# Kernel tuning notes

Hardware: AMD Instinct MI355X
Metric: run time of the kernel (lower is better)

The kernel has to match this reference:

```python
import jax, jax.numpy as jnp
import numpy as np

NUM_HEADS = 16
NUM_KV_HEADS = 4
HEAD_DIM = 128
ROPE_THETA = 10000.0


def _rope_cos_sin(T, dim, theta):
    inv_freq = 1.0 / (theta ** (jnp.arange(0, dim, 2, dtype=jnp.float32) / dim))
    freqs = jnp.arange(T, dtype=jnp.float32)[:, None] * inv_freq[None, :]  # (T, dim/2)
    emb = jnp.concatenate([freqs, freqs], axis=-1)  # (T, dim)
    return jnp.cos(emb), jnp.sin(emb)


def _rotate_half(x):
    h = x.shape[-1] // 2
    return jnp.concatenate([-x[..., h:], x[..., :h]], axis=-1)


def _apply_rope(x, cos, sin):
    # x: (B, H, T, D); cos/sin: (T, D)
    return x * cos[None, None] + _rotate_half(x) * sin[None, None]


def setup_inputs() -> dict:
    key = jax.random.key(0)
    ks = jax.random.split(key, 6)
    B, T, H = 2, 2048, 2048
    latent = 256
    kv_dim = NUM_KV_HEADS * HEAD_DIM
    s = 0.02
    return {
        "x": jax.random.normal(ks[0], (B, T, H), jnp.float32),
        "wq": jax.random.normal(ks[1], (H, H), jnp.float32) * s,
        "wkv": jax.random.normal(ks[2], (latent, H), jnp.float32) * s,
        "wk": jax.random.normal(ks[3], (kv_dim, latent), jnp.float32) * s,
        "wv": jax.random.normal(ks[4], (kv_dim, latent), jnp.float32) * s,
        "wo": jax.random.normal(ks[5], (H, H), jnp.float32) * s,
    }


def reference(x, wq, wkv, wk, wv, wo):
    B, T, hidden = x.shape
    nh, nkv, hd = NUM_HEADS, NUM_KV_HEADS, HEAD_DIM

    q = jnp.einsum('bth,dh->btd', x, wq)
    kv_latent = jnp.einsum('bth,lh->btl', x, wkv)
    k = jnp.einsum('btl,dl->btd', kv_latent, wk)
    v = jnp.einsum('btl,dl->btd', kv_latent, wv)

    q = q.reshape(B, T, nh, hd).transpose(0, 2, 1, 3)   # (B, nh, T, hd)
    k = k.reshape(B, T, nkv, hd).transpose(0, 2, 1, 3)  # (B, nkv, T, hd)
    v = v.reshape(B, T, nkv, hd).transpose(0, 2, 1, 3)

    cos, sin = _rope_cos_sin(T, hd, ROPE_THETA)
    q = _apply_rope(q, cos, sin)
    k = _apply_rope(k, cos, sin)

    rep = nh // nkv
    k = jnp.repeat(k, rep, axis=1)  # (B, nh, T, hd)
    v = jnp.repeat(v, rep, axis=1)

    scores = jnp.einsum('bhqd,bhkd->bhqk', q, k) * (1.0 / np.sqrt(hd))
    causal = jnp.triu(jnp.ones((T, T), dtype=bool), k=1)
    scores = jnp.where(causal[None, None], -jnp.inf, scores)
    probs = jax.nn.softmax(scores, axis=-1)
    out = jnp.einsum('bhqk,bhkd->bhqd', probs, v)
    out = out.transpose(0, 2, 1, 3).reshape(B, T, nh * hd)
    return jnp.einsum('btd,hd->bth', out, wo)
```

## Files before the change

### kernel.cpp

```cpp
#include <hip/hip_runtime.h>
#include <hip/hip_bf16.h>
#include <math.h>


#define AS1 __attribute__((address_space(1)))
#define AS3 __attribute__((address_space(3)))
#define QSTRIDE 2304

typedef short bf16x8 __attribute__((ext_vector_type(8)));
typedef float f32x4 __attribute__((ext_vector_type(4)));
typedef float f32x16 __attribute__((ext_vector_type(16)));
typedef unsigned int uint32x2 __attribute__((ext_vector_type(2)));

__device__ __forceinline__ unsigned short f2bf(float x) {
  union { float f; unsigned int u; } q; q.f = x;
  unsigned int u = q.u;
  u += 0x7FFFu + ((u >> 16) & 1u);
  return (unsigned short)(u >> 16);
}
__device__ __forceinline__ float bf2f(unsigned short x) {
  union { unsigned int u; float f; } q; q.u = ((unsigned int)x) << 16;
  return q.f;
}
__device__ __forceinline__ unsigned int pack2bf(float a, float b) {
  return (unsigned int)f2bf(a) | ((unsigned int)f2bf(b) << 16);
}
__device__ __forceinline__ unsigned int pack2bf_hw(float a, float b) {
  __hip_bfloat162 h = __float22bfloat162_rn(make_float2(a, b));
  union { __hip_bfloat162 h; unsigned int u; } c; c.h = h;
  return c.u;
}
__device__ __forceinline__ uint32x2 plswap(unsigned int a, unsigned int b) {
  return __builtin_amdgcn_permlane32_swap(a, b, false, false);
}
__device__ __forceinline__ float xor32_add(float x) {
  union { float f; unsigned int u; } X; X.f = x;
  uint32x2 r = plswap(X.u, X.u);
  union { unsigned int u; float f; } A, B; A.u = r.x; B.u = r.y;
  return A.f + B.f;
}

__global__ __launch_bounds__(256) void rope_table(float* __restrict__ cost,
                                                  float* __restrict__ sint,
                                                  int T) {
  int idx = blockIdx.x * 256 + threadIdx.x;
  if (idx >= T * 64) return;
  int t = idx >> 6, j = idx & 63;
  double invf = pow(10000.0, -(double)j / 64.0);
  double ang = (double)t * invf;
  cost[idx] = (float)cos(ang);
  sint[idx] = (float)sin(ang);
}

__global__ __launch_bounds__(256) void conv_bf16(const float* __restrict__ src,
                                                 unsigned short* __restrict__ dst,
                                                 int n) {
  int i = (blockIdx.x * 256 + threadIdx.x) * 4;
  if (i >= n) return;
  float4 f = *(const float4*)(src + i);
  ushort4 o;
  o.x = f2bf(f.x); o.y = f2bf(f.y); o.z = f2bf(f.z); o.w = f2bf(f.w);
  *(ushort4*)(dst + i) = o;
}

template <bool OUT_BF16>
__global__ __launch_bounds__(256) void gemm_mfma(const unsigned short* __restrict__ A,
                                                 const unsigned short* __restrict__ W,
                                                 void* __restrict__ Cv,
                                                 int M, int N, int K,
                                                 int lda, int ldw, int ldc,
                                                 int nwgx) {
  __shared__ unsigned short Asl[2][128 * 32];
  __shared__ unsigned short Wsl[2][128 * 32];
  int tid = threadIdx.x;
  int w = tid >> 6, lane = tid & 63;
  int g = lane >> 4, c = lane & 15;
  int wm = w >> 1, wn = w & 1;

  int nwg = gridDim.x;
  int cpx = nwg >> 3;
  int orig = blockIdx.x;
  int swz = (orig & 7) * cpx + (orig >> 3);
  int m0 = (swz / nwgx) * 128, n0 = (swz % nwgx) * 128;

  f32x4 acc[4][4] = {};

#pragma unroll
  for (int i = 0; i < 2; ++i) {
    int idx = i * 256 + tid;
    int row = idx >> 2;
    int kk = (idx & 3) * 8;
    __builtin_amdgcn_global_load_lds(
        (const AS1 void*)(A + (size_t)(m0 + row) * lda + kk),
        (AS3 void*)(Asl[0] + ((size_t)i * 256 + (w << 6)) * 8), 16, 0, 0);
    __builtin_amdgcn_global_load_lds(
        (const AS1 void*)(W + (size_t)(n0 + row) * ldw + kk),
        (AS3 void*)(Wsl[0] + ((size_t)i * 256 + (w << 6)) * 8), 16, 0, 0);
  }
  __syncthreads();

  int cur = 0;
  for (int k0 = 0; k0 < K; k0 += 32) {
    if (k0 + 32 < K) {
      int nb = cur ^ 1;
#pragma unroll
      for (int i = 0; i < 2; ++i) {
        int idx = i * 256 + tid;
        int row = idx >> 2;
        int kk = (idx & 3) * 8;
        __builtin_amdgcn_global_load_lds(
            (const AS1 void*)(A + (size_t)(m0 + row) * lda + k0 + 32 + kk),
            (AS3 void*)(Asl[nb] + ((size_t)i * 256 + (w << 6)) * 8), 16, 0, 0);
        __builtin_amdgcn_global_load_lds(
            (const AS1 void*)(W + (size_t)(n0 + row) * ldw + k0 + 32 + kk),
            (AS3 void*)(Wsl[nb] + ((size_t)i * 256 + (w << 6)) * 8), 16, 0, 0);
      }
    }
    bf16x8 af[4], wf[4];
#pragma unroll
    for (int mi = 0; mi < 4; ++mi)
      af[mi] = *(const bf16x8*)(Asl[cur] + (wm * 64 + mi * 16 + c) * 32 + g * 8);
#pragma unroll
    for (int ni = 0; ni < 4; ++ni)
      wf[ni] = *(const bf16x8*)(Wsl[cur] + (wn * 64 + ni * 16 + c) * 32 + g * 8);
#pragma unroll
    for (int mi = 0; mi < 4; ++mi)
#pragma unroll
      for (int ni = 0; ni < 4; ++ni)
        acc[mi][ni] = __builtin_amdgcn_mfma_f32_16x16x32_bf16(af[mi], wf[ni],
                                                              acc[mi][ni], 0, 0, 0);
    __syncthreads();
    cur ^= 1;
  }
#pragma unroll
  for (int mi = 0; mi < 4; ++mi)
#pragma unroll
    for (int r = 0; r < 4; ++r) {
      size_t mrow = (size_t)(m0 + wm * 64 + mi * 16 + g * 4 + r) * ldc;
#pragma unroll
      for (int ni = 0; ni < 4; ++ni) {
        int n = n0 + wn * 64 + ni * 16 + c;
        if (OUT_BF16)
          ((unsigned short*)Cv)[mrow + n] = f2bf(acc[mi][ni][r]);
        else
          ((float*)Cv)[mrow + n] = acc[mi][ni][r];
      }
    }
}

__global__ __launch_bounds__(256) void rope_ip_bf16(unsigned short* __restrict__ buf,
                                                    int nheads, int T, int rowstride,
                                                    const float* __restrict__ cost,
                                                    const float* __restrict__ sint,
                                                    float scale) {
  int idx = blockIdx.x * 256 + threadIdx.x;
  int d = idx & 63;
  int rest = idx >> 6;
  int h = rest % nheads;
  int bt = rest / nheads;
  int t = bt & (T - 1);
  unsigned short* p = buf + (size_t)bt * rowstride + h * 128;
  float cc = cost[t * 64 + d], ss = sint[t * 64 + d];
  float x0 = bf2f(p[d]), x1 = bf2f(p[d + 64]);
  p[d]      = f2bf((x0 * cc - x1 * ss) * scale);
  p[d + 64] = f2bf((x1 * cc + x0 * ss) * scale);
}

__global__ __launch_bounds__(256) void rope_pack_k(const unsigned short* __restrict__ kvcat,
                                                   unsigned short* __restrict__ kp,
                                                   const float* __restrict__ cost,
                                                   const float* __restrict__ sint) {
  int idx = blockIdx.x * 256 + threadIdx.x;
  int d = idx & 63;
  int rest = idx >> 6;
  int kvh = rest & 3;
  int bt = rest >> 2;
  int t = bt & 2047, b = bt >> 11;
  const unsigned short* src = kvcat + (size_t)bt * 1024 + kvh * 128;
  float cc = cost[t * 64 + d], ss = sint[t * 64 + d];
  float x0 = bf2f(src[d]), x1 = bf2f(src[d + 64]);
  unsigned short y0 = f2bf(x0 * cc - x1 * ss);
  unsigned short y1 = f2bf(x1 * cc + x0 * ss);
  int kr = t & 31;
  size_t base = (size_t)(b * 4 + kvh) * 262144 + (size_t)(t >> 5) * 4096;
  kp[base + ((kr * 128 + d)      ^ ((kr & 7) << 3))] = y0;
  kp[base + ((kr * 128 + d + 64) ^ ((kr & 7) << 3))] = y1;
}

__global__ __launch_bounds__(256) void transpose_v(const unsigned short* __restrict__ kvcat,
                                                   unsigned short* __restrict__ vp) {
  __shared__ unsigned short tile[32][33];
  int t0 = blockIdx.x * 32, d0 = blockIdx.y * 32, b = blockIdx.z;
  int tx = threadIdx.x & 31, ty = threadIdx.x >> 5;
#pragma unroll
  for (int i = 0; i < 4; ++i) {
    int t = ty + i * 8;
    tile[t][tx] = kvcat[((size_t)(b * 2048 + t0 + t)) * 1024 + 512 + d0 + tx];
  }
  __syncthreads();
#pragma unroll
  for (int i = 0; i < 4; ++i) {
    int dd = ty + i * 8;
    int D = d0 + dd;
    int d = D & 127;
    int t = t0 + tx;
    size_t base = (size_t)(b * 4 + (D >> 7)) * 262144 + (size_t)(t >> 5) * 4096;
    vp[base + ((d * 32 + (t & 31)) ^ ((d & 3) << 3))] = tile[tx][dd];
  }
}

__global__ __launch_bounds__(256, 2) void attn_mfma(const unsigned short* __restrict__ qb,
                                                    const unsigned short* __restrict__ kp,
                                                    const unsigned short* __restrict__ vp,
                                                    unsigned short* __restrict__ attob) {
  __shared__ unsigned short smem[16896];

  int tid = threadIdx.x;
  int w = tid >> 6, lane = tid & 63;
  int wq = w >> 1, wk = w & 1;
  int cl = lane & 31, hi = lane >> 5;
  int stream = blockIdx.x & 31;
  int G = 31 - (blockIdx.x >> 5);
  int h = stream & 15, b = stream >> 4;
  int kvh = h >> 2;
  int q0w = G * 64 + wq * 32;
  int nt = 2 * G + 2;

  const unsigned short* kpS = kp + (size_t)(b * 4 + kvh) * 262144;
  const unsigned short* vpS = vp + (size_t)(b * 4 + kvh) * 262144;

  bf16x8 qa[8];
  {
    const unsigned short* qrow = qb + ((size_t)(b * 2048 + q0w + cl)) * QSTRIDE + h * 128 + hi * 8;
#pragma unroll
    for (int kc = 0; kc < 8; ++kc)
      qa[kc] = *(const bf16x8*)(qrow + kc * 16);
  }

  f32x16 o0 = {}, o1 = {}, o2 = {}, o3 = {};
  float l = 0.f;

#pragma unroll
  for (int i = 0; i < 2; ++i) {
    __builtin_amdgcn_global_load_lds(
        (const AS1 void*)(kpS + (size_t)w * 1024 + i * 512 + lane * 8),
        (AS3 void*)(&smem[w * 1024 + i * 512]), 16, 0, 0);
    __builtin_amdgcn_global_load_lds(
        (const AS1 void*)(vpS + (size_t)w * 1024 + i * 512 + lane * 8),
        (AS3 void*)(&smem[8192 + w * 1024 + i * 512]), 16, 0, 0);
  }
  __syncthreads();

  int cur = 0;
  for (int ti = 0; ti < nt; ++ti) {
    if (ti + 1 < nt) {
      size_t src = (size_t)(ti + 1) * 4096 + w * 1024 + lane * 8;
      int nb = cur ^ 1;
#pragma unroll
      for (int i = 0; i < 2; ++i) {
        __builtin_amdgcn_global_load_lds(
            (const AS1 void*)(kpS + src + i * 512),
            (AS3 void*)(&smem[nb * 4096 + w * 1024 + i * 512]), 16, 0, 0);
        __builtin_amdgcn_global_load_lds(
            (const AS1 void*)(vpS + src + i * 512),
            (AS3 void*)(&smem[8192 + nb * 4096 + w * 1024 + i * 512]), 16, 0, 0);
      }
    }
    int ks0 = ti << 5;
    if (((ti & 1) == wk) && (ks0 <= q0w)) {
      const unsigned short* kb_ = &smem[cur * 4096];
      const unsigned short* vb_ = &smem[8192 + cur * 4096];
      bf16x8 kf[8];
#pragma unroll
      for (int kc = 0; kc < 8; ++kc)
        kf[kc] = *(const bf16x8*)&kb_[(cl * 128 + kc * 16 + hi * 8) ^ ((cl & 7) << 3)];
      f32x16 sA = {}, sB = {};
      __builtin_amdgcn_s_setprio(1);
#pragma unroll
      for (int kc = 0; kc < 4; ++kc) {
        sA = __builtin_amdgcn_mfma_f32_32x32x16_bf16(kf[kc * 2],     qa[kc * 2],     sA, 0, 0, 0);
        sB = __builtin_amdgcn_mfma_f32_32x32x16_bf16(kf[kc * 2 + 1], qa[kc * 2 + 1], sB, 0, 0, 0);
      }
      __builtin_amdgcn_s_setprio(0);
      f32x16 sS = sA + sB;
      bf16x8 vf[8];
#pragma unroll
      for (int db = 0; db < 4; ++db)
#pragma unroll
        for (int ks = 0; ks < 2; ++ks)
          vf[db * 2 + ks] = *(const bf16x8*)&vb_[((db * 32 + cl) * 32
                              + ks * 16 + hi * 8) ^ ((cl & 3) << 3)];
      if (ks0 == q0w) {
#pragma unroll
        for (int r = 0; r < 16; ++r) {
          int krow = (r & 3) + 8 * (r >> 2) + 4 * hi;
          if (krow > cl) sS[r] = -INFINITY;
        }
      }
      float p[16];
#pragma unroll
      for (int r = 0; r < 16; ++r) p[r] = __expf(sS[r]);
      float rs = ((p[0] + p[1]) + (p[2] + p[3])) + ((p[4] + p[5]) + (p[6] + p[7]))
               + ((p[8] + p[9]) + (p[10] + p[11])) + ((p[12] + p[13]) + (p[14] + p[15]));
      l += rs;
      union { unsigned int u[4]; bf16x8 v; } pb0, pb1;
      {
        uint32x2 r0 = plswap(pack2bf_hw(p[0], p[1]), pack2bf_hw(p[4], p[5]));
        uint32x2 r1 = plswap(pack2bf_hw(p[2], p[3]), pack2bf_hw(p[6], p[7]));
        pb0.u[0] = r0.x; pb0.u[1] = r1.x; pb0.u[2] = r0.y; pb0.u[3] = r1.y;
        uint32x2 r2 = plswap(pack2bf_hw(p[8], p[9]), pack2bf_hw(p[12], p[13]));
        uint32x2 r3 = plswap(pack2bf_hw(p[10], p[11]), pack2bf_hw(p[14], p[15]));
        pb1.u[0] = r2.x; pb1.u[1] = r3.x; pb1.u[2] = r2.y; pb1.u[3] = r3.y;
      }
      __builtin_amdgcn_s_setprio(1);
      o0 = __builtin_amdgcn_mfma_f32_32x32x16_bf16(vf[0], pb0.v, o0, 0, 0, 0);
      o1 = __builtin_amdgcn_mfma_f32_32x32x16_bf16(vf[2], pb0.v, o1, 0, 0, 0);
      o2 = __builtin_amdgcn_mfma_f32_32x32x16_bf16(vf[4], pb0.v, o2, 0, 0, 0);
      o3 = __builtin_amdgcn_mfma_f32_32x32x16_bf16(vf[6], pb0.v, o3, 0, 0, 0);
      o0 = __builtin_amdgcn_mfma_f32_32x32x16_bf16(vf[1], pb1.v, o0, 0, 0, 0);
      o1 = __builtin_amdgcn_mfma_f32_32x32x16_bf16(vf[3], pb1.v, o1, 0, 0, 0);
      o2 = __builtin_amdgcn_mfma_f32_32x32x16_bf16(vf[5], pb1.v, o2, 0, 0, 0);
      o3 = __builtin_amdgcn_mfma_f32_32x32x16_bf16(vf[7], pb1.v, o3, 0, 0, 0);
      __builtin_amdgcn_s_setprio(0);
    }
    __syncthreads();
    cur ^= 1;
  }

  float lsum = xor32_add(l);
  float* lptr = (float*)&smem[16384];
  int qr = wq * 32 + cl;
  if (hi == 0) lptr[wk * 64 + qr] = lsum;
#pragma unroll
  for (int r = 0; r < 16; ++r) {
    int dl = (r & 3) + 8 * (r >> 2) + 4 * hi;
    smem[wk * 8192 + qr * 128 + dl]      = f2bf(o0[r]);
    smem[wk * 8192 + qr * 128 + 32 + dl] = f2bf(o1[r]);
    smem[wk * 8192 + qr * 128 + 64 + dl] = f2bf(o2[r]);
    smem[wk * 8192 + qr * 128 + 96 + dl] = f2bf(o3[r]);
  }
  __syncthreads();

  {
    int q = tid >> 2;
    int dc = (tid & 3) * 32;
    float inv = 1.f / (lptr[q] + lptr[64 + q]);
    unsigned short* orow = attob + ((size_t)(b * 2048 + G * 64 + q)) * 2048 + h * 128 + dc;
#pragma unroll
    for (int i4 = 0; i4 < 4; ++i4) {
      bf16x8 a = *(const bf16x8*)&smem[q * 128 + dc + i4 * 8];
      bf16x8 c = *(const bf16x8*)&smem[8192 + q * 128 + dc + i4 * 8];
      union { unsigned int u[4]; bf16x8 v; } ov;
#pragma unroll
      for (int j = 0; j < 4; ++j) {
        float s0 = (bf2f((unsigned short)a[j * 2])     + bf2f((unsigned short)c[j * 2]))     * inv;
        float s1 = (bf2f((unsigned short)a[j * 2 + 1]) + bf2f((unsigned short)c[j * 2 + 1])) * inv;
        ov.u[j] = pack2bf(s0, s1);
      }
      *(bf16x8*)(orow + i4 * 8) = ov.v;
    }
  }
}

extern "C" void kernel_launch(void* const* d_in, const int* in_sizes, int n_in,
                              void* d_out, int out_size, void* d_ws, size_t ws_size,
                              hipStream_t stream) {
  const float* x   = (const float*)d_in[0];
  const float* wq  = (const float*)d_in[1];
  const float* wkv = (const float*)d_in[2];
  const float* wk  = (const float*)d_in[3];
  const float* wv  = (const float*)d_in[4];
  const float* wo  = (const float*)d_in[5];
  float* out = (float*)d_out;
  float* ws  = (float*)d_ws;

  const int B = 2, T = 2048, H = 2048, NH = 16, NKV = 4, LAT = 256, KVD = 512;
  const int BT = B * T;

  size_t off = 0;
  unsigned short* xb    = (unsigned short*)(ws + off); off += (size_t)BT * H / 2;
  unsigned short* wqb   = (unsigned short*)(ws + off); off += (size_t)H * H / 2;
  unsigned short* wkvb  = (unsigned short*)(ws + off); off += (size_t)LAT * H / 2;
  unsigned short* wkb   = (unsigned short*)(ws + off); off += (size_t)KVD * LAT / 2;
  unsigned short* wvb   = (unsigned short*)(ws + off); off += (size_t)KVD * LAT / 2;
  unsigned short* wob   = (unsigned short*)(ws + off); off += (size_t)H * H / 2;
  unsigned short* qkv   = (unsigned short*)(ws + off); off += (size_t)BT * QSTRIDE / 2;
  unsigned short* kvcat = (unsigned short*)(ws + off); off += (size_t)BT * 1024 / 2;
  unsigned short* kp    = (unsigned short*)(ws + off); off += (size_t)BT * KVD / 2;
  unsigned short* vp    = (unsigned short*)(ws + off); off += (size_t)BT * KVD / 2;
  unsigned short* attob = (unsigned short*)(ws + off); off += (size_t)BT * H / 2;
  float* cost = ws + off; off += (size_t)T * 64;
  float* sint = ws + off; off += (size_t)T * 64;

  const float scale = 0.088388347648318447f;

  rope_table<<<(T * 64 + 255) / 256, 256, 0, stream>>>(cost, sint, T);

  conv_bf16<<<(BT * H / 4) / 256, 256, 0, stream>>>(x, xb, BT * H);
  conv_bf16<<<(H * H / 4) / 256, 256, 0, stream>>>(wq, wqb, H * H);
  conv_bf16<<<(LAT * H / 4) / 256, 256, 0, stream>>>(wkv, wkvb, LAT * H);
  conv_bf16<<<(KVD * LAT / 4) / 256, 256, 0, stream>>>(wk, wkb, KVD * LAT);
  conv_bf16<<<(KVD * LAT / 4) / 256, 256, 0, stream>>>(wv, wvb, KVD * LAT);
  conv_bf16<<<(H * H / 4) / 256, 256, 0, stream>>>(wo, wob, H * H);

  gemm_mfma<true><<<(QSTRIDE / 128) * (BT / 128), 256, 0, stream>>>(
      xb, wqb, qkv, BT, QSTRIDE, H, H, H, QSTRIDE, QSTRIDE / 128);
  gemm_mfma<true><<<(1024 / 128) * (BT / 128), 256, 0, stream>>>(
      qkv + H, wkb, kvcat, BT, 1024, LAT, QSTRIDE, LAT, 1024, 1024 / 128);

  rope_ip_bf16<<<(BT * NH * 64) / 256, 256, 0, stream>>>(qkv, NH, T, QSTRIDE, cost, sint, scale);
  rope_pack_k<<<(BT * NKV * 64) / 256, 256, 0, stream>>>(kvcat, kp, cost, sint);
  transpose_v<<<dim3(T / 32, KVD / 32, B), 256, 0, stream>>>(kvcat, vp);

  attn_mfma<<<1024, 256, 0, stream>>>(qkv, kp, vp, attob);

  gemm_mfma<false><<<(H / 128) * (BT / 128), 256, 0, stream>>>(
      attob, wob, out, BT, H, H, H, H, H, H / 128);
}
```

Before: 223.1 us.

## Split attention key range into two halves and add a combine kernel

Each attention query block's key tiles are split into two halves handled by separate blocks, doubling the grid from 1024 to 2048. Each half writes unnormalized bf16 partial outputs and row sums into dead workspace regions (the xb/weights area and kvcat). A new combine kernel adds the two partials and divides by the summed row sums to produce attob. The aim is better load balance and occupancy on the causal triangle, at the cost of an extra launch, extra global traffic for the partials, and an extra bf16 rounding step.

```diff
diff --git a/kernel.cpp b/kernel.cpp
--- a/kernel.cpp
+++ b/kernel.cpp
@@ -212,19 +212,25 @@
 __global__ __launch_bounds__(256, 2) void attn_mfma(const unsigned short* __restrict__ qb,
                                                     const unsigned short* __restrict__ kp,
                                                     const unsigned short* __restrict__ vp,
-                                                    unsigned short* __restrict__ attob) {
+                                                    unsigned short* __restrict__ partA,
+                                                    unsigned short* __restrict__ partB,
+                                                    float* __restrict__ lpart) {
   __shared__ unsigned short smem[16896];
 
   int tid = threadIdx.x;
   int w = tid >> 6, lane = tid & 63;
   int wq = w >> 1, wk = w & 1;
   int cl = lane & 31, hi = lane >> 5;
-  int stream = blockIdx.x & 31;
-  int G = 31 - (blockIdx.x >> 5);
+  int bid = blockIdx.x;
+  int stream = bid & 31;
+  int rest = bid >> 5;
+  int G = 31 - (rest >> 1);
+  int half = rest & 1;
   int h = stream & 15, b = stream >> 4;
   int kvh = h >> 2;
   int q0w = G * 64 + wq * 32;
-  int nt = 2 * G + 2;
+  int tstart = half ? (G + 1) : 0;
+  int tend = half ? (2 * G + 2) : (G + 1);
 
   const unsigned short* kpS = kp + (size_t)(b * 4 + kvh) * 262144;
   const unsigned short* vpS = vp + (size_t)(b * 4 + kvh) * 262144;
@@ -242,18 +248,19 @@
 
 #pragma unroll
   for (int i = 0; i < 2; ++i) {
+    size_t src = (size_t)tstart * 4096 + w * 1024 + i * 512 + lane * 8;
     __builtin_amdgcn_global_load_lds(
-        (const AS1 void*)(kpS + (size_t)w * 1024 + i * 512 + lane * 8),
+        (const AS1 void*)(kpS + src),
         (AS3 void*)(&smem[w * 1024 + i * 512]), 16, 0, 0);
     __builtin_amdgcn_global_load_lds(
-        (const AS1 void*)(vpS + (size_t)w * 1024 + i * 512 + lane * 8),
+        (const AS1 void*)(vpS + src),
         (AS3 void*)(&smem[8192 + w * 1024 + i * 512]), 16, 0, 0);
   }
   __syncthreads();
 
   int cur = 0;
-  for (int ti = 0; ti < nt; ++ti) {
-    if (ti + 1 < nt) {
+  for (int ti = tstart; ti < tend; ++ti) {
+    if (ti + 1 < tend) {
       size_t src = (size_t)(ti + 1) * 4096 + w * 1024 + lane * 8;
       int nb = cur ^ 1;
 #pragma unroll
@@ -342,10 +349,11 @@
   __syncthreads();
 
   {
+    unsigned short* op = (bid < 1600) ? (partA + (size_t)bid * 8192)
+                                      : (partB + (size_t)(bid - 1600) * 8192);
     int q = tid >> 2;
     int dc = (tid & 3) * 32;
-    float inv = 1.f / (lptr[q] + lptr[64 + q]);
-    unsigned short* orow = attob + ((size_t)(b * 2048 + G * 64 + q)) * 2048 + h * 128 + dc;
+    if ((tid & 3) == 0) lpart[(size_t)bid * 64 + q] = lptr[q] + lptr[64 + q];
 #pragma unroll
     for (int i4 = 0; i4 < 4; ++i4) {
       bf16x8 a = *(const bf16x8*)&smem[q * 128 + dc + i4 * 8];
@@ -353,12 +361,47 @@
       union { unsigned int u[4]; bf16x8 v; } ov;
 #pragma unroll
       for (int j = 0; j < 4; ++j) {
-        float s0 = (bf2f((unsigned short)a[j * 2])     + bf2f((unsigned short)c[j * 2]))     * inv;
-        float s1 = (bf2f((unsigned short)a[j * 2 + 1]) + bf2f((unsigned short)c[j * 2 + 1])) * inv;
+        float s0 = bf2f((unsigned short)a[j * 2])     + bf2f((unsigned short)c[j * 2]);
+        float s1 = bf2f((unsigned short)a[j * 2 + 1]) + bf2f((unsigned short)c[j * 2 + 1]);
         ov.u[j] = pack2bf(s0, s1);
       }
-      *(bf16x8*)(orow + i4 * 8) = ov.v;
-    }
+      *(bf16x8*)(op + q * 128 + dc + i4 * 8) = ov.v;
+    }
+  }
+}
+
+__global__ __launch_bounds__(256) void attn_combine(const unsigned short* __restrict__ partA,
+                                                    const unsigned short* __restrict__ partB,
+                                                    const float* __restrict__ lpart,
+                                                    unsigned short* __restrict__ attob) {
+  int id = blockIdx.x;
+  int stream = id & 31;
+  int rest2 = id >> 5;
+  int G = 31 - rest2;
+  int h = stream & 15, b = stream >> 4;
+  int p0 = (2 * rest2) * 32 + stream;
+  int p1 = p0 + 32;
+  const unsigned short* o0 = (p0 < 1600) ? (partA + (size_t)p0 * 8192)
+                                         : (partB + (size_t)(p0 - 1600) * 8192);
+  const unsigned short* o1 = (p1 < 1600) ? (partA + (size_t)p1 * 8192)
+                                         : (partB + (size_t)(p1 - 1600) * 8192);
+  int tid = threadIdx.x;
+  int q = tid >> 2;
+  int dc = (tid & 3) * 32;
+  float inv = 1.f / (lpart[(size_t)p0 * 64 + q] + lpart[(size_t)p1 * 64 + q]);
+  unsigned short* orow = attob + ((size_t)(b * 2048 + G * 64 + q)) * 2048 + h * 128 + dc;
+#pragma unroll
+  for (int i4 = 0; i4 < 4; ++i4) {
+    bf16x8 a = *(const bf16x8*)(o0 + q * 128 + dc + i4 * 8);
+    bf16x8 c = *(const bf16x8*)(o1 + q * 128 + dc + i4 * 8);
+    union { unsigned int u[4]; bf16x8 v; } ov;
+#pragma unroll
+    for (int j = 0; j < 4; ++j) {
+      float s0 = (bf2f((unsigned short)a[j * 2])     + bf2f((unsigned short)c[j * 2]))     * inv;
+      float s1 = (bf2f((unsigned short)a[j * 2 + 1]) + bf2f((unsigned short)c[j * 2 + 1])) * inv;
+      ov.u[j] = pack2bf(s0, s1);
+    }
+    *(bf16x8*)(orow + i4 * 8) = ov.v;
   }
 }
 
@@ -392,6 +435,10 @@
   float* cost = ws + off; off += (size_t)T * 64;
   float* sint = ws + off; off += (size_t)T * 64;
 
+  unsigned short* partA = (unsigned short*)ws;
+  unsigned short* partB = kvcat;
+  float* lpart = (float*)(kvcat + (size_t)448 * 8192);
+
   const float scale = 0.088388347648318447f;
 
   rope_table<<<(T * 64 + 255) / 256, 256, 0, stream>>>(cost, sint, T);
@@ -412,7 +459,8 @@
   rope_pack_k<<<(BT * NKV * 64) / 256, 256, 0, stream>>>(kvcat, kp, cost, sint);
   transpose_v<<<dim3(T / 32, KVD / 32, B), 256, 0, stream>>>(kvcat, vp);
 
-  attn_mfma<<<1024, 256, 0, stream>>>(qkv, kp, vp, attob);
+  attn_mfma<<<2048, 256, 0, stream>>>(qkv, kp, vp, partA, partB, lpart);
+  attn_combine<<<1024, 256, 0, stream>>>(partA, partB, lpart, attob);
 
   gemm_mfma<false><<<(H / 128) * (BT / 128), 256, 0, stream>>>(
       attob, wob, out, BT, H, H, H, H, H, H / 128);
```

New measurement: 256.2 us. 14.8% more time.
